# Kernel optimization log

Measured on AMD Instinct MI355X. Metric: run time of the kernel, lower is better.

Reference implementation:

```python
import jax, jax.numpy as jnp
import numpy as np

B, S, D, F, K = 32, 512, 256, 256, 3

def setup_inputs() -> dict:
    key = jax.random.key(0)
    ks = jax.random.split(key, 8)
    x = jax.random.normal(ks[0], (B, S, D), dtype=jnp.float32)
    target = jax.random.uniform(ks[1], (B, S), dtype=jnp.float32, minval=1.0, maxval=8.0)
    expand_max_len = int(jnp.round(target.sum(-1)).max())
    sc = 0.05
    conv1_w = jax.random.normal(ks[2], (F, D, K), dtype=jnp.float32) * sc
    conv1_b = jnp.zeros((F,), jnp.float32)
    conv2_w = jax.random.normal(ks[3], (F, F, K), dtype=jnp.float32) * sc
    conv2_b = jnp.zeros((F,), jnp.float32)
    norm1_g = jnp.ones((F,), jnp.float32); norm1_b = jnp.zeros((F,), jnp.float32)
    norm2_g = jnp.ones((F,), jnp.float32); norm2_b = jnp.zeros((F,), jnp.float32)
    lin_w = jax.random.normal(ks[4], (F,), dtype=jnp.float32) * sc
    lin_b = jnp.zeros((), jnp.float32)
    return {"x": x, "target": target, "conv1_w": conv1_w, "conv1_b": conv1_b,
            "conv2_w": conv2_w, "conv2_b": conv2_b, "norm1_g": norm1_g, "norm1_b": norm1_b,
            "norm2_g": norm2_g, "norm2_b": norm2_b, "lin_w": lin_w, "lin_b": lin_b,
            "expand_max_len": expand_max_len}

def _layernorm(h, g, b, eps=1e-5):
    mu = jnp.mean(h, axis=-1, keepdims=True)
    var = jnp.mean((h - mu) ** 2, axis=-1, keepdims=True)
    return (h - mu) * jax.lax.rsqrt(var + eps) * g + b

def _conv1d(h_bsd, w, bias):
    # h_bsd: [B,S,C] -> conv over time with 'same' padding -> [B,S,F]
    h = jnp.transpose(h_bsd, (0, 2, 1))  # [B,C,S]
    out = jax.lax.conv_general_dilated(h, w, window_strides=(1,),
                                       padding=[(K // 2, K // 2)],
                                       dimension_numbers=("NCH", "OIH", "NCH"))
    out = out + bias[None, :, None]
    return jnp.transpose(out, (0, 2, 1))  # [B,S,F]

def _duration_predict(x, conv1_w, conv1_b, conv2_w, conv2_b,
                      norm1_g, norm1_b, norm2_g, norm2_b, lin_w, lin_b):
    h = _conv1d(x, conv1_w, conv1_b)
    h = jax.nn.relu(_layernorm(h, norm1_g, norm1_b))  # dropout is identity in eval
    h = _conv1d(h, conv2_w, conv2_b)
    h = jax.nn.relu(_layernorm(h, norm2_g, norm2_b))
    return jax.nn.relu(h @ lin_w + lin_b)  # [B,S]

def _length_regulate(x, target, L):
    d = jnp.round(target)                # [B,S] integer-valued durations
    ends = jnp.cumsum(d, axis=-1)        # [B,S]
    starts = ends - d
    t = jnp.arange(L, dtype=d.dtype)     # [L]
    mask = ((t[None, None, :] >= starts[:, :, None]) &
            (t[None, None, :] < ends[:, :, None])).astype(x.dtype)  # [B,S,L]
    # x^T @ mask -> [B,D,L]; return transposed [B,L,D]
    return jnp.einsum("bsd,bsl->bld", x, mask)

def reference(x, target, conv1_w, conv1_b, conv2_w, conv2_b,
              norm1_g, norm1_b, norm2_g, norm2_b, lin_w, lin_b, expand_max_len):
    predicted_len = _duration_predict(x, conv1_w, conv1_b, conv2_w, conv2_b,
                                      norm1_g, norm1_b, norm2_g, norm2_b, lin_w, lin_b)
    output = _length_regulate(x, target, expand_max_len)
    return (output, predicted_len)
```

## Files before the change

kernel.cpp:

```cpp
#include <hip/hip_runtime.h>
#include <hip/hip_bf16.h>

#define NB 32
#define NS 512
#define NC 256
#define NKSTEP 24
#define ROWS 32
#define HALO_ROWS 34

typedef __attribute__((ext_vector_type(8))) short short8;
typedef __attribute__((ext_vector_type(4))) float f32x4;

__device__ __forceinline__ unsigned pack2(float a, float b) {
    __hip_bfloat16 ha = __float2bfloat16(a), hb = __float2bfloat16(b);
    return ((unsigned)(*(unsigned short*)&hb) << 16) | (unsigned)(*(unsigned short*)&ha);
}

__global__ __launch_bounds__(256) void prep_and_scan(
    const float* __restrict__ w1, const float* __restrict__ w2,
    unsigned short* __restrict__ Bp1, unsigned short* __restrict__ Bp2,
    const float* __restrict__ target, int* __restrict__ idx, int L)
{
    __shared__ int bufa[512], bufb[512];
    const int t = threadIdx.x;

    if (blockIdx.x < 512) {
        const bool second = blockIdx.x >= 256;
        const int f = blockIdx.x & 255;
        const float* w = second ? w2 : w1;
        unsigned short* Bp = second ? Bp2 : Bp1;
        const float* wf = w + (size_t)f * 768 + t * 3;
        const float v[3] = {wf[0], wf[1], wf[2]};
#pragma unroll
        for (int shift = 0; shift < 3; ++shift) {
            const int k = shift * 256 + t;
            const int o = f * 32 + (k >> 5) * 8192 + (k & 31);
            __hip_bfloat16 h = __float2bfloat16(v[shift]);
            Bp[o] = *(unsigned short*)&h;
        }
        return;
    }

    const int b = blockIdx.x - 512;
    const float* tb = target + (size_t)b * NS;
    const int d0 = (int)rintf(tb[t]);
    const int d1 = (int)rintf(tb[t + 256]);
    bufa[t] = d0; bufa[t + 256] = d1;
    __syncthreads();
    int* src = bufa;
    int* dst = bufb;
    for (int off = 1; off < 512; off <<= 1) {
        for (int i = t; i < 512; i += 256) {
            int v = src[i];
            if (i >= off) v += src[i - off];
            dst[i] = v;
        }
        __syncthreads();
        int* tmp = src; src = dst; dst = tmp;
    }
    const int e0 = src[t], e1 = src[t + 256], total = src[511];
    int* ib = idx + (size_t)b * L;
    const int hi0 = e0 < L ? e0 : L;
    const int hi1 = e1 < L ? e1 : L;
    for (int k = e0 - d0; k < hi0; ++k) ib[k] = t;
    for (int k = e1 - d1; k < hi1; ++k) ib[k] = t + 256;
    for (int k = total + t; k < L; k += 256) ib[k] = -1;
}

template <bool FINAL, typename Tin>
__global__ __launch_bounds__(256, 4) void conv_mfma(
    const Tin* __restrict__ in,
    const uint4* __restrict__ Bp,
    const float* __restrict__ bias,
    const float* __restrict__ gamma,
    const float* __restrict__ beta,
    const float* __restrict__ linw,
    const float* __restrict__ linb,
    void* __restrict__ outp)
{
    __shared__ __align__(16) uint4 xs[HALO_ROWS * 32];
    __shared__ float red[ROWS][4][2];
    __shared__ float dotb[ROWS][4];

    const int tid = threadIdx.x;
    const int b   = blockIdx.x >> 4;
    const int s0  = (blockIdx.x & 15) << 5;

    {
        const int slot = tid & 31;
        for (int r = tid >> 5; r < HALO_ROWS; r += 8) {
            const int s = s0 - 1 + r;
            uint4 v = {0u, 0u, 0u, 0u};
            if (s >= 0 && s < NS) {
                if constexpr (sizeof(Tin) == 4) {
                    const float* src = (const float*)in + ((size_t)(b * NS + s)) * NC + slot * 8;
                    const float4 lo = *(const float4*)src;
                    const float4 hi = *(const float4*)(src + 4);
                    v.x = pack2(lo.x, lo.y); v.y = pack2(lo.z, lo.w);
                    v.z = pack2(hi.x, hi.y); v.w = pack2(hi.z, hi.w);
                } else {
                    v = *(const uint4*)((const unsigned short*)in +
                                        ((size_t)(b * NS + s)) * NC + slot * 8);
                }
            }
            xs[r * 32 + (slot ^ ((r & 7) << 2))] = v;
        }
    }
    __syncthreads();

    const int lane = tid & 63;
    const int w    = tid >> 6;
    const int n0   = w << 6;
    const int l15  = lane & 15;
    const int lg   = lane >> 4;

    f32x4 acc[2][4];
#pragma unroll
    for (int mi = 0; mi < 2; ++mi)
#pragma unroll
        for (int ni = 0; ni < 4; ++ni) acc[mi][ni] = (f32x4){0.f, 0.f, 0.f, 0.f};

    const uint4* bbase = Bp + (size_t)(n0 + l15) * 4 + lg;

    auto lda = [&](int ks, int mi) -> short8 {
        const int row  = mi * 16 + l15 + (ks >> 3);
        int slot = ((ks & 7) << 2) + lg;
        slot ^= (row & 7) << 2;
        return *(const short8*)&xs[row * 32 + slot];
    };
    auto ldb = [&](int ks, int ni) -> short8 {
        return *(const short8*)(const void*)(bbase + ks * 1024 + ni * 64);
    };

    short8 areg[2][2], breg[2][4];
#pragma unroll
    for (int q = 0; q < 2; ++q) {
#pragma unroll
        for (int ni = 0; ni < 4; ++ni) breg[q][ni] = ldb(q, ni);
#pragma unroll
        for (int mi = 0; mi < 2; ++mi) areg[q][mi] = lda(q, mi);
    }

#pragma unroll
    for (int p = 0; p < NKSTEP; ++p) {
        const int rs = p & 1;
#pragma unroll
        for (int mi = 0; mi < 2; ++mi)
#pragma unroll
            for (int ni = 0; ni < 4; ++ni)
                acc[mi][ni] = __builtin_amdgcn_mfma_f32_16x16x32_bf16(
                    areg[rs][mi], breg[rs][ni], acc[mi][ni], 0, 0, 0);
        if (p + 2 < NKSTEP) {
#pragma unroll
            for (int ni = 0; ni < 4; ++ni) breg[rs][ni] = ldb(p + 2, ni);
#pragma unroll
            for (int mi = 0; mi < 2; ++mi) areg[rs][mi] = lda(p + 2, mi);
        }
    }

    float bv[4], gv[4], bt[4], lwv[4];
#pragma unroll
    for (int ni = 0; ni < 4; ++ni) {
        const int col = n0 + ni * 16 + l15;
        bv[ni] = bias[col]; gv[ni] = gamma[col]; bt[ni] = beta[col];
        if constexpr (FINAL) lwv[ni] = linw[col];
    }
#pragma unroll
    for (int mi = 0; mi < 2; ++mi)
#pragma unroll
        for (int ni = 0; ni < 4; ++ni)
#pragma unroll
            for (int i = 0; i < 4; ++i) acc[mi][ni][i] += bv[ni];

#pragma unroll
    for (int mi = 0; mi < 2; ++mi) {
        float s[4] = {0, 0, 0, 0}, q[4] = {0, 0, 0, 0};
#pragma unroll
        for (int ni = 0; ni < 4; ++ni)
#pragma unroll
            for (int i = 0; i < 4; ++i) {
                const float v = acc[mi][ni][i];
                s[i] += v; q[i] += v * v;
            }
#pragma unroll
        for (int i = 0; i < 4; ++i)
#pragma unroll
            for (int m = 1; m < 16; m <<= 1) {
                s[i] += __shfl_xor(s[i], m, 64);
                q[i] += __shfl_xor(q[i], m, 64);
            }
        if (l15 == 0) {
#pragma unroll
            for (int i = 0; i < 4; ++i) {
                red[mi * 16 + lg * 4 + i][w][0] = s[i];
                red[mi * 16 + lg * 4 + i][w][1] = q[i];
            }
        }
    }
    __syncthreads();

#pragma unroll
    for (int mi = 0; mi < 2; ++mi) {
#pragma unroll
        for (int i = 0; i < 4; ++i) {
            const int row = mi * 16 + lg * 4 + i;
            float sum = 0.f, sq = 0.f;
#pragma unroll
            for (int ww = 0; ww < 4; ++ww) { sum += red[row][ww][0]; sq += red[row][ww][1]; }
            const float mu = sum * (1.f / 256.f);
            const float rs = rsqrtf(sq * (1.f / 256.f) - mu * mu + 1e-5f);
            float p = 0.f;
#pragma unroll
            for (int ni = 0; ni < 4; ++ni) {
                const float y = fmaxf(0.f, (acc[mi][ni][i] - mu) * rs * gv[ni] + bt[ni]);
                if constexpr (!FINAL) {
                    __hip_bfloat16 h = __float2bfloat16(y);
                    ((unsigned short*)outp)[((size_t)(b * NS + s0 + row)) * NC +
                                            n0 + ni * 16 + l15] = *(unsigned short*)&h;
                } else {
                    p += y * lwv[ni];
                }
            }
            if constexpr (FINAL) {
#pragma unroll
                for (int m = 1; m < 16; m <<= 1) p += __shfl_xor(p, m, 64);
                if (l15 == 0) dotb[row][w] = p;
            }
        }
    }
    if constexpr (FINAL) {
        __syncthreads();
        if (tid < ROWS) {
            const float tot = dotb[tid][0] + dotb[tid][1] + dotb[tid][2] + dotb[tid][3] + linb[0];
            ((float*)outp)[b * NS + s0 + tid] = fmaxf(0.f, tot);
        }
    }
}

__global__ __launch_bounds__(256) void gather2(const float4* __restrict__ x4,
                                               const int* __restrict__ idx,
                                               float4* __restrict__ out4, int L)
{
    const int b    = blockIdx.y;
    const int f0   = blockIdx.x * 8 + (threadIdx.x >> 6) * 2;
    const int lane = threadIdx.x & 63;
#pragma unroll
    for (int j = 0; j < 2; ++j) {
        const int frame = f0 + j;
        if (frame >= L) return;
        const int pos = idx[(size_t)b * L + frame];
        float4 v = {0.f, 0.f, 0.f, 0.f};
        if (pos >= 0) v = x4[(((size_t)(b * NS + pos)) << 6) + lane];
        out4[(((size_t)b * L + frame) << 6) + lane] = v;
    }
}

extern "C" void kernel_launch(void* const* d_in, const int* in_sizes, int n_in,
                              void* d_out, int out_size, void* d_ws, size_t ws_size,
                              hipStream_t stream)
{
    const float* x    = (const float*)d_in[0];
    const float* targ = (const float*)d_in[1];
    const float* c1w  = (const float*)d_in[2];
    const float* c1b  = (const float*)d_in[3];
    const float* c2w  = (const float*)d_in[4];
    const float* c2b  = (const float*)d_in[5];
    const float* n1g  = (const float*)d_in[6];
    const float* n1b  = (const float*)d_in[7];
    const float* n2g  = (const float*)d_in[8];
    const float* n2b  = (const float*)d_in[9];
    const float* lw   = (const float*)d_in[10];
    const float* lb   = (const float*)d_in[11];

    const int L = (out_size - NB * NS) / (NB * NC);

    unsigned short* Bp1 = (unsigned short*)d_ws;
    unsigned short* Bp2 = Bp1 + 196608;
    unsigned short* h1  = Bp2 + 196608;
    int* idx = (int*)(h1 + (size_t)NB * NS * NC);
    float* out  = (float*)d_out;
    float* pred = out + (size_t)NB * (size_t)L * NC;

    prep_and_scan<<<dim3(512 + NB), 256, 0, stream>>>(c1w, c2w, Bp1, Bp2, targ, idx, L);

    conv_mfma<false, float><<<dim3(NB * 16), 256, 0, stream>>>(
        x, (const uint4*)Bp1, c1b, n1g, n1b, nullptr, nullptr, (void*)h1);
    conv_mfma<true, unsigned short><<<dim3(NB * 16), 256, 0, stream>>>(
        h1, (const uint4*)Bp2, c2b, n2g, n2b, lw, lb, (void*)pred);

    gather2<<<dim3((L + 7) / 8, NB), 256, 0, stream>>>(
        (const float4*)x, idx, (float4*)out, L);
}
```

Measured before the change: 158.7 us.

## Fuse both conv layers with halo recompute and merge gather into one launch

Merges the two conv+layernorm kernels into a single kernel. Each block computes 32 rows of the first conv, covering 30 output rows plus a halo, and keeps them in LDS as bf16 for the second conv. This removes the global round-trip of the intermediate activation and one launch. The gather blocks are appended to the same grid, so the memory-bound expansion overlaps with the compute-bound conv blocks and another launch disappears. The cost is about 7% redundant conv1 work from halo recompute, plus extra LDS use (16KB more) that may lower occupancy.

```diff
diff --git a/kernel.cpp b/kernel.cpp
--- a/kernel.cpp
+++ b/kernel.cpp
@@ -5,8 +5,11 @@
 #define NS 512
 #define NC 256
 #define NKSTEP 24
-#define ROWS 32
-#define HALO_ROWS 34
+#define TROWS 30
+#define NT 18
+#define HROWS 32
+#define XROWS 34
+#define CONV_BLOCKS (NB * NT)
 
 typedef __attribute__((ext_vector_type(8))) short short8;
 typedef __attribute__((ext_vector_type(4))) float f32x4;
@@ -67,41 +70,54 @@
     for (int k = total + t; k < L; k += 256) ib[k] = -1;
 }
 
-template <bool FINAL, typename Tin>
-__global__ __launch_bounds__(256, 4) void conv_mfma(
-    const Tin* __restrict__ in,
-    const uint4* __restrict__ Bp,
-    const float* __restrict__ bias,
-    const float* __restrict__ gamma,
-    const float* __restrict__ beta,
-    const float* __restrict__ linw,
-    const float* __restrict__ linb,
-    void* __restrict__ outp)
+__global__ __launch_bounds__(256, 4) void fused_conv_gather(
+    const float* __restrict__ x,
+    const uint4* __restrict__ Bp1, const uint4* __restrict__ Bp2,
+    const float* __restrict__ bias1, const float* __restrict__ g1, const float* __restrict__ be1,
+    const float* __restrict__ bias2, const float* __restrict__ g2, const float* __restrict__ be2,
+    const float* __restrict__ linw, const float* __restrict__ linb,
+    const int* __restrict__ idx, float* __restrict__ pred,
+    const float4* __restrict__ x4, float4* __restrict__ out4, int L)
 {
-    __shared__ __align__(16) uint4 xs[HALO_ROWS * 32];
-    __shared__ float red[ROWS][4][2];
-    __shared__ float dotb[ROWS][4];
+    __shared__ __align__(16) uint4 xs[XROWS * 32];
+    __shared__ __align__(16) unsigned short hs[HROWS * 256];
+    __shared__ float red[HROWS][4][2];
+    __shared__ float dotb[HROWS][4];
 
     const int tid = threadIdx.x;
-    const int b   = blockIdx.x >> 4;
-    const int s0  = (blockIdx.x & 15) << 5;
+
+    if (blockIdx.x >= CONV_BLOCKS) {
+        const int g    = blockIdx.x - CONV_BLOCKS;
+        const int b    = g & 31;
+        const int f0   = (g >> 5) * 8 + (tid >> 6) * 2;
+        const int lane = tid & 63;
+#pragma unroll
+        for (int j = 0; j < 2; ++j) {
+            const int frame = f0 + j;
+            if (frame >= L) break;
+            const int pos = idx[(size_t)b * L + frame];
+            float4 v = {0.f, 0.f, 0.f, 0.f};
+            if (pos >= 0) v = x4[(((size_t)(b * NS + pos)) << 6) + lane];
+            out4[(((size_t)b * L + frame) << 6) + lane] = v;
+        }
+        return;
+    }
+
+    const int b  = blockIdx.x / NT;
+    const int t  = blockIdx.x - b * NT;
+    const int s0 = t * TROWS;
 
     {
         const int slot = tid & 31;
-        for (int r = tid >> 5; r < HALO_ROWS; r += 8) {
-            const int s = s0 - 1 + r;
+        for (int r = tid >> 5; r < XROWS; r += 8) {
+            const int s = s0 - 2 + r;
             uint4 v = {0u, 0u, 0u, 0u};
             if (s >= 0 && s < NS) {
-                if constexpr (sizeof(Tin) == 4) {
-                    const float* src = (const float*)in + ((size_t)(b * NS + s)) * NC + slot * 8;
-                    const float4 lo = *(const float4*)src;
-                    const float4 hi = *(const float4*)(src + 4);
-                    v.x = pack2(lo.x, lo.y); v.y = pack2(lo.z, lo.w);
-                    v.z = pack2(hi.x, hi.y); v.w = pack2(hi.z, hi.w);
-                } else {
-                    v = *(const uint4*)((const unsigned short*)in +
-                                        ((size_t)(b * NS + s)) * NC + slot * 8);
-                }
+                const float* src = x + ((size_t)(b * NS + s)) * NC + slot * 8;
+                const float4 lo = *(const float4*)src;
+                const float4 hi = *(const float4*)(src + 4);
+                v.x = pack2(lo.x, lo.y); v.y = pack2(lo.z, lo.w);
+                v.z = pack2(hi.x, hi.y); v.w = pack2(hi.z, hi.w);
             }
             xs[r * 32 + (slot ^ ((r & 7) << 2))] = v;
         }
@@ -114,33 +130,36 @@
     const int l15  = lane & 15;
     const int lg   = lane >> 4;
 
-    f32x4 acc[2][4];
-#pragma unroll
-    for (int mi = 0; mi < 2; ++mi)
-#pragma unroll
-        for (int ni = 0; ni < 4; ++ni) acc[mi][ni] = (f32x4){0.f, 0.f, 0.f, 0.f};
-
-    const uint4* bbase = Bp + (size_t)(n0 + l15) * 4 + lg;
-
-    auto lda = [&](int ks, int mi) -> short8 {
-        const int row  = mi * 16 + l15 + (ks >> 3);
+    auto ldax = [&](int ks, int mi) -> short8 {
+        const int row = mi * 16 + l15 + (ks >> 3);
         int slot = ((ks & 7) << 2) + lg;
         slot ^= (row & 7) << 2;
         return *(const short8*)&xs[row * 32 + slot];
     };
-    auto ldb = [&](int ks, int ni) -> short8 {
-        return *(const short8*)(const void*)(bbase + ks * 1024 + ni * 64);
+    auto ldah = [&](int ks, int mi) -> short8 {
+        const int row = mi * 16 + l15 + (ks >> 3);
+        int slot = ((ks & 7) << 2) + lg;
+        slot ^= (row & 7) << 2;
+        return *(const short8*)&hs[row * 256 + slot * 8];
     };
 
+    const uint4* bb1 = Bp1 + (size_t)(n0 + l15) * 4 + lg;
+    const uint4* bb2 = Bp2 + (size_t)(n0 + l15) * 4 + lg;
+
+    f32x4 acc[2][4];
     short8 areg[2][2], breg[2][4];
+
+#pragma unroll
+    for (int mi = 0; mi < 2; ++mi)
+#pragma unroll
+        for (int ni = 0; ni < 4; ++ni) acc[mi][ni] = (f32x4){0.f, 0.f, 0.f, 0.f};
 #pragma unroll
     for (int q = 0; q < 2; ++q) {
 #pragma unroll
-        for (int ni = 0; ni < 4; ++ni) breg[q][ni] = ldb(q, ni);
-#pragma unroll
-        for (int mi = 0; mi < 2; ++mi) areg[q][mi] = lda(q, mi);
-    }
-
+        for (int ni = 0; ni < 4; ++ni) breg[q][ni] = *(const short8*)(const void*)(bb1 + q * 1024 + ni * 64);
+#pragma unroll
+        for (int mi = 0; mi < 2; ++mi) areg[q][mi] = ldax(q, mi);
+    }
 #pragma unroll
     for (int p = 0; p < NKSTEP; ++p) {
         const int rs = p & 1;
@@ -152,106 +171,164 @@
                     areg[rs][mi], breg[rs][ni], acc[mi][ni], 0, 0, 0);
         if (p + 2 < NKSTEP) {
 #pragma unroll
-            for (int ni = 0; ni < 4; ++ni) breg[rs][ni] = ldb(p + 2, ni);
-#pragma unroll
-            for (int mi = 0; mi < 2; ++mi) areg[rs][mi] = lda(p + 2, mi);
-        }
-    }
-
-    float bv[4], gv[4], bt[4], lwv[4];
-#pragma unroll
-    for (int ni = 0; ni < 4; ++ni) {
-        const int col = n0 + ni * 16 + l15;
-        bv[ni] = bias[col]; gv[ni] = gamma[col]; bt[ni] = beta[col];
-        if constexpr (FINAL) lwv[ni] = linw[col];
-    }
+            for (int ni = 0; ni < 4; ++ni) breg[rs][ni] = *(const short8*)(const void*)(bb1 + (p + 2) * 1024 + ni * 64);
+#pragma unroll
+            for (int mi = 0; mi < 2; ++mi) areg[rs][mi] = ldax(p + 2, mi);
+        }
+    }
+
+    {
+        float bv[4];
+#pragma unroll
+        for (int ni = 0; ni < 4; ++ni) bv[ni] = bias1[n0 + ni * 16 + l15];
+#pragma unroll
+        for (int mi = 0; mi < 2; ++mi) {
+            float s[4] = {0, 0, 0, 0}, q[4] = {0, 0, 0, 0};
+#pragma unroll
+            for (int ni = 0; ni < 4; ++ni)
+#pragma unroll
+                for (int i = 0; i < 4; ++i) {
+                    const float v = (acc[mi][ni][i] += bv[ni]);
+                    s[i] += v; q[i] += v * v;
+                }
+#pragma unroll
+            for (int i = 0; i < 4; ++i)
+#pragma unroll
+                for (int m = 1; m < 16; m <<= 1) {
+                    s[i] += __shfl_xor(s[i], m, 64);
+                    q[i] += __shfl_xor(q[i], m, 64);
+                }
+            if (l15 == 0) {
+#pragma unroll
+                for (int i = 0; i < 4; ++i) {
+                    red[mi * 16 + lg * 4 + i][w][0] = s[i];
+                    red[mi * 16 + lg * 4 + i][w][1] = q[i];
+                }
+            }
+        }
+    }
+    __syncthreads();
+
+    {
+        float gv[4], bt[4];
+#pragma unroll
+        for (int ni = 0; ni < 4; ++ni) { gv[ni] = g1[n0 + ni * 16 + l15]; bt[ni] = be1[n0 + ni * 16 + l15]; }
+#pragma unroll
+        for (int mi = 0; mi < 2; ++mi)
+#pragma unroll
+            for (int i = 0; i < 4; ++i) {
+                const int row = mi * 16 + lg * 4 + i;
+                const int sh  = s0 - 1 + row;
+                const bool ok = (sh >= 0) && (sh < NS);
+                float sum = 0.f, sq = 0.f;
+#pragma unroll
+                for (int ww = 0; ww < 4; ++ww) { sum += red[row][ww][0]; sq += red[row][ww][1]; }
+                const float mu = sum * (1.f / 256.f);
+                const float rs = rsqrtf(sq * (1.f / 256.f) - mu * mu + 1e-5f);
+#pragma unroll
+                for (int ni = 0; ni < 4; ++ni) {
+                    const int col = n0 + ni * 16 + l15;
+                    float y = fmaxf(0.f, (acc[mi][ni][i] - mu) * rs * gv[ni] + bt[ni]);
+                    if (!ok) y = 0.f;
+                    __hip_bfloat16 hv = __float2bfloat16(y);
+                    const int slot = (col >> 3) ^ ((row & 7) << 2);
+                    hs[row * 256 + slot * 8 + (col & 7)] = *(unsigned short*)&hv;
+                }
+            }
+    }
+    __syncthreads();
+
 #pragma unroll
     for (int mi = 0; mi < 2; ++mi)
 #pragma unroll
-        for (int ni = 0; ni < 4; ++ni)
-#pragma unroll
-            for (int i = 0; i < 4; ++i) acc[mi][ni][i] += bv[ni];
-
-#pragma unroll
-    for (int mi = 0; mi < 2; ++mi) {
-        float s[4] = {0, 0, 0, 0}, q[4] = {0, 0, 0, 0};
-#pragma unroll
-        for (int ni = 0; ni < 4; ++ni)
+        for (int ni = 0; ni < 4; ++ni) acc[mi][ni] = (f32x4){0.f, 0.f, 0.f, 0.f};
+#pragma unroll
+    for (int q = 0; q < 2; ++q) {
+#pragma unroll
+        for (int ni = 0; ni < 4; ++ni) breg[q][ni] = *(const short8*)(const void*)(bb2 + q * 1024 + ni * 64);
+#pragma unroll
+        for (int mi = 0; mi < 2; ++mi) areg[q][mi] = ldah(q, mi);
+    }
+#pragma unroll
+    for (int p = 0; p < NKSTEP; ++p) {
+        const int rs = p & 1;
+#pragma unroll
+        for (int mi = 0; mi < 2; ++mi)
+#pragma unroll
+            for (int ni = 0; ni < 4; ++ni)
+                acc[mi][ni] = __builtin_amdgcn_mfma_f32_16x16x32_bf16(
+                    areg[rs][mi], breg[rs][ni], acc[mi][ni], 0, 0, 0);
+        if (p + 2 < NKSTEP) {
+#pragma unroll
+            for (int ni = 0; ni < 4; ++ni) breg[rs][ni] = *(const short8*)(const void*)(bb2 + (p + 2) * 1024 + ni * 64);
+#pragma unroll
+            for (int mi = 0; mi < 2; ++mi) areg[rs][mi] = ldah(p + 2, mi);
+        }
+    }
+
+    {
+        float bv[4];
+#pragma unroll
+        for (int ni = 0; ni < 4; ++ni) bv[ni] = bias2[n0 + ni * 16 + l15];
+#pragma unroll
+        for (int mi = 0; mi < 2; ++mi) {
+            float s[4] = {0, 0, 0, 0}, q[4] = {0, 0, 0, 0};
+#pragma unroll
+            for (int ni = 0; ni < 4; ++ni)
+#pragma unroll
+                for (int i = 0; i < 4; ++i) {
+                    const float v = (acc[mi][ni][i] += bv[ni]);
+                    s[i] += v; q[i] += v * v;
+                }
+#pragma unroll
+            for (int i = 0; i < 4; ++i)
+#pragma unroll
+                for (int m = 1; m < 16; m <<= 1) {
+                    s[i] += __shfl_xor(s[i], m, 64);
+                    q[i] += __shfl_xor(q[i], m, 64);
+                }
+            if (l15 == 0) {
+#pragma unroll
+                for (int i = 0; i < 4; ++i) {
+                    red[mi * 16 + lg * 4 + i][w][0] = s[i];
+                    red[mi * 16 + lg * 4 + i][w][1] = q[i];
+                }
+            }
+        }
+    }
+    __syncthreads();
+
+    {
+        float gv[4], bt[4], lwv[4];
+#pragma unroll
+        for (int ni = 0; ni < 4; ++ni) {
+            const int col = n0 + ni * 16 + l15;
+            gv[ni] = g2[col]; bt[ni] = be2[col]; lwv[ni] = linw[col];
+        }
+#pragma unroll
+        for (int mi = 0; mi < 2; ++mi)
 #pragma unroll
             for (int i = 0; i < 4; ++i) {
-                const float v = acc[mi][ni][i];
-                s[i] += v; q[i] += v * v;
-            }
-#pragma unroll
-        for (int i = 0; i < 4; ++i)
-#pragma unroll
-            for (int m = 1; m < 16; m <<= 1) {
-                s[i] += __shfl_xor(s[i], m, 64);
-                q[i] += __shfl_xor(q[i], m, 64);
-            }
-        if (l15 == 0) {
-#pragma unroll
-            for (int i = 0; i < 4; ++i) {
-                red[mi * 16 + lg * 4 + i][w][0] = s[i];
-                red[mi * 16 + lg * 4 + i][w][1] = q[i];
-            }
-        }
-    }
-    __syncthreads();
-
-#pragma unroll
-    for (int mi = 0; mi < 2; ++mi) {
-#pragma unroll
-        for (int i = 0; i < 4; ++i) {
-            const int row = mi * 16 + lg * 4 + i;
-            float sum = 0.f, sq = 0.f;
-#pragma unroll
-            for (int ww = 0; ww < 4; ++ww) { sum += red[row][ww][0]; sq += red[row][ww][1]; }
-            const float mu = sum * (1.f / 256.f);
-            const float rs = rsqrtf(sq * (1.f / 256.f) - mu * mu + 1e-5f);
-            float p = 0.f;
-#pragma unroll
-            for (int ni = 0; ni < 4; ++ni) {
-                const float y = fmaxf(0.f, (acc[mi][ni][i] - mu) * rs * gv[ni] + bt[ni]);
-                if constexpr (!FINAL) {
-                    __hip_bfloat16 h = __float2bfloat16(y);
-                    ((unsigned short*)outp)[((size_t)(b * NS + s0 + row)) * NC +
-                                            n0 + ni * 16 + l15] = *(unsigned short*)&h;
-                } else {
-                    p += y * lwv[ni];
-                }
-            }
-            if constexpr (FINAL) {
+                const int row = mi * 16 + lg * 4 + i;
+                float sum = 0.f, sq = 0.f;
+#pragma unroll
+                for (int ww = 0; ww < 4; ++ww) { sum += red[row][ww][0]; sq += red[row][ww][1]; }
+                const float mu = sum * (1.f / 256.f);
+                const float rs = rsqrtf(sq * (1.f / 256.f) - mu * mu + 1e-5f);
+                float p = 0.f;
+#pragma unroll
+                for (int ni = 0; ni < 4; ++ni)
+                    p += fmaxf(0.f, (acc[mi][ni][i] - mu) * rs * gv[ni] + bt[ni]) * lwv[ni];
 #pragma unroll
                 for (int m = 1; m < 16; m <<= 1) p += __shfl_xor(p, m, 64);
                 if (l15 == 0) dotb[row][w] = p;
             }
-        }
-    }
-    if constexpr (FINAL) {
-        __syncthreads();
-        if (tid < ROWS) {
-            const float tot = dotb[tid][0] + dotb[tid][1] + dotb[tid][2] + dotb[tid][3] + linb[0];
-            ((float*)outp)[b * NS + s0 + tid] = fmaxf(0.f, tot);
-        }
-    }
-}
-
-__global__ __launch_bounds__(256) void gather2(const float4* __restrict__ x4,
-                                               const int* __restrict__ idx,
-                                               float4* __restrict__ out4, int L)
-{
-    const int b    = blockIdx.y;
-    const int f0   = blockIdx.x * 8 + (threadIdx.x >> 6) * 2;
-    const int lane = threadIdx.x & 63;
-#pragma unroll
-    for (int j = 0; j < 2; ++j) {
-        const int frame = f0 + j;
-        if (frame >= L) return;
-        const int pos = idx[(size_t)b * L + frame];
-        float4 v = {0.f, 0.f, 0.f, 0.f};
-        if (pos >= 0) v = x4[(((size_t)(b * NS + pos)) << 6) + lane];
-        out4[(((size_t)b * L + frame) << 6) + lane] = v;
+    }
+    __syncthreads();
+
+    if (tid < TROWS && s0 + tid < NS) {
+        const float tot = dotb[tid][0] + dotb[tid][1] + dotb[tid][2] + dotb[tid][3] + linb[0];
+        pred[b * NS + s0 + tid] = fmaxf(0.f, tot);
     }
 }
 
@@ -276,18 +353,15 @@
 
     unsigned short* Bp1 = (unsigned short*)d_ws;
     unsigned short* Bp2 = Bp1 + 196608;
-    unsigned short* h1  = Bp2 + 196608;
-    int* idx = (int*)(h1 + (size_t)NB * NS * NC);
+    int* idx = (int*)(Bp2 + 196608);
     float* out  = (float*)d_out;
     float* pred = out + (size_t)NB * (size_t)L * NC;
 
     prep_and_scan<<<dim3(512 + NB), 256, 0, stream>>>(c1w, c2w, Bp1, Bp2, targ, idx, L);
 
-    conv_mfma<false, float><<<dim3(NB * 16), 256, 0, stream>>>(
-        x, (const uint4*)Bp1, c1b, n1g, n1b, nullptr, nullptr, (void*)h1);
-    conv_mfma<true, unsigned short><<<dim3(NB * 16), 256, 0, stream>>>(
-        h1, (const uint4*)Bp2, c2b, n2g, n2b, lw, lb, (void*)pred);
-
-    gather2<<<dim3((L + 7) / 8, NB), 256, 0, stream>>>(
-        (const float4*)x, idx, (float4*)out, L);
+    const int nfb = (L + 7) / 8;
+    fused_conv_gather<<<dim3(CONV_BLOCKS + NB * nfb), 256, 0, stream>>>(
+        x, (const uint4*)Bp1, (const uint4*)Bp2,
+        c1b, n1g, n1b, c2b, n2g, n2b, lw, lb,
+        idx, pred, (const float4*)x, (float4*)out, L);
 }
```

Result: faster. 154.0 us (-3.0%).
